# Performance work log

Hardware: AMD Instinct MI355X
Metric: run time of the kernel (lower is better)

## Reference

```python
import jax, jax.numpy as jnp
import numpy as np
from jax import lax

SEQ, B, IN, H, NLAYERS, OUT_LEN, OUT_SIZE = 80, 32768, 2, 10, 2, 20, 2


def _lstm_layer(x, h0, c0, Wih, Whh, bih, bhh):
    """PyTorch-convention LSTM layer. x: [T,B,F], h0/c0: [B,H]. Returns [T,B,H]."""
    b = bih + bhh  # [4H]

    def step(carry, xt):
        h, c = carry
        gates = xt @ Wih.T + h @ Whh.T + b  # [B,4H], gate order i,f,g,o
        i, f, g, o = jnp.split(gates, 4, axis=-1)
        i = jax.nn.sigmoid(i)
        f = jax.nn.sigmoid(f)
        g = jnp.tanh(g)
        o = jax.nn.sigmoid(o)
        c = f * c + i * g
        h = o * jnp.tanh(c)
        return (h, c), h

    (_, _), ys = lax.scan(step, (h0, c0), x)
    return ys


def setup_inputs() -> dict:
    key = jax.random.key(0)
    ks = jax.random.split(key, 16)
    s = 1.0 / np.sqrt(H)  # torch default init scale
    u = lambda k, shp: jax.random.uniform(k, shp, jnp.float32, -s, s)
    inp = {
        "x": jax.random.normal(ks[0], (SEQ, B, IN), jnp.float32),
        "h0": jnp.zeros((NLAYERS, B, H), jnp.float32),
        "c0": jnp.zeros((NLAYERS, B, H), jnp.float32),
        # layer 0 LSTM params
        "Wih0": u(ks[1], (4 * H, IN)),
        "Whh0": u(ks[2], (4 * H, H)),
        "bih0": u(ks[3], (4 * H,)),
        "bhh0": u(ks[4], (4 * H,)),
        # layer 1 LSTM params
        "Wih1": u(ks[5], (4 * H, H)),
        "Whh1": u(ks[6], (4 * H, H)),
        "bih1": u(ks[7], (4 * H,)),
        "bhh1": u(ks[8], (4 * H,)),
        # MLP head: Linear(800 -> 10), Sigmoid, Linear(10 -> 40)
        "W1": jax.random.uniform(ks[9], (H, SEQ * H), jnp.float32, -1 / np.sqrt(SEQ * H), 1 / np.sqrt(SEQ * H)),
        "b1": jax.random.uniform(ks[10], (H,), jnp.float32, -1 / np.sqrt(SEQ * H), 1 / np.sqrt(SEQ * H)),
        "W2": u(ks[11], (OUT_LEN * OUT_SIZE, H)),
        "b2": u(ks[12], (OUT_LEN * OUT_SIZE,)),
    }
    return inp


def reference(x, h0, c0, Wih0, Whh0, bih0, bhh0, Wih1, Whh1, bih1, bhh1, W1, b1, W2, b2):
    y0 = _lstm_layer(x, h0[0], c0[0], Wih0, Whh0, bih0, bhh0)   # [T,B,H]
    y1 = _lstm_layer(y0, h0[1], c0[1], Wih1, Whh1, bih1, bhh1)  # [T,B,H]
    out = jnp.tanh(y1)
    out = out.reshape(B, -1)  # faithful to torch .view(batch, -1) on [T,B,H]
    out = jax.nn.sigmoid(out @ W1.T + b1)
    out = out @ W2.T + b2  # [B, OUT_LEN*OUT_SIZE]
    return out.reshape(OUT_LEN, B, OUT_SIZE)
```

## Files before the change

kernel.cpp:

```cpp
#include <hip/hip_runtime.h>
#include <hip/hip_fp16.h>

#define SEQ   80
#define BATCH 32768
#define HID   10

typedef unsigned int uint;
typedef unsigned short ushort;
typedef _Float16 f16;
typedef __attribute__((ext_vector_type(8))) _Float16 f16x8;
typedef __attribute__((ext_vector_type(2))) _Float16 f16x2;
typedef __attribute__((ext_vector_type(4))) float f32x4;

#define SIG_SCALE  (-1.44269504f)
#define TANH_SCALE (-2.88539008f)

__device__ __forceinline__ float fast_rcp(float x)  { return __builtin_amdgcn_rcpf(x); }
__device__ __forceinline__ float fast_exp2(float x) { return __builtin_amdgcn_exp2f(x); }
__device__ __forceinline__ float sigp(float a)  { return fast_rcp(1.0f + fast_exp2(a)); }
__device__ __forceinline__ float tanhp(float a) { return 2.0f * fast_rcp(1.0f + fast_exp2(a)) - 1.0f; }
__device__ __forceinline__ float tanh_f(float x){ return tanhp(TANH_SCALE * x); }

union U4V { uint4 u; f16x8 v; };
union UH2 { uint u; f16x2 h; };
union HU  { f16 h; ushort s; };

__device__ __forceinline__ float lstm_unit(const f32x4 d, float& c) {
    const float Ei = fast_exp2(d[0]);
    const float Ef = fast_exp2(d[1]);
    const float Eg = fast_exp2(d[2]);
    const float Eo = fast_exp2(d[3]);
    const float Rf  = fast_rcp(1.0f + Ef);
    const float Rig = fast_rcp((1.0f + Ei) * (1.0f + Eg));
    c = c * Rf + (1.0f - Eg) * Rig;
    const float Ec = fast_exp2(TANH_SCALE * c);
    const float Rh = fast_rcp((1.0f + Eo) * (1.0f + Ec));
    return (1.0f - Ec) * Rh;
}

__global__ __launch_bounds__(256, 2)
void lstm2_mfma(const float* __restrict__ x, const float* __restrict__ h0in,
                const float* __restrict__ c0in,
                const float* __restrict__ Wih0, const float* __restrict__ Whh0,
                const float* __restrict__ bih0, const float* __restrict__ bhh0,
                const float* __restrict__ Wih1, const float* __restrict__ Whh1,
                const float* __restrict__ bih1, const float* __restrict__ bhh1,
                ushort* __restrict__ y ) {
    __shared__ char lds_all[4 * 16 * 80];
    const int tid = threadIdx.x;
    const int l   = tid & 63;
    const int wv  = tid >> 6;
    char* lds   = lds_all + wv * (16 * 80);
    const int bl  = l & 15;
    const int grp = l >> 4;
    const long b  = ((long)blockIdx.x * 4 + wv) * 16 + bl;

    f16x8 A0[3], A1[3];
    f32x4 bs0[3], bs1[3];
#pragma unroll
    for (int T = 0; T < 3; ++T) {
        const int R  = 16 * T + bl;
        const int u  = R >> 2, gi = R & 3;
        const bool vr = (R < 40);
        const int tr = gi * 10 + u;
        const float sc = (gi == 2) ? TANH_SCALE : SIG_SCALE;
#pragma unroll
        for (int j = 0; j < 8; ++j) {
            const int k = grp * 8 + j;
            float w0 = 0.f, w1 = 0.f;
            if (vr) {
                if (k < 10)      w0 = Whh0[tr * 10 + k];
                else if (k < 12) w0 = Wih0[tr * 2 + (k - 10)];
                if (k < 10)      w1 = Wih1[tr * 10 + k];
                else if (k < 20) w1 = Whh1[tr * 10 + (k - 10)];
            }
            A0[T][j] = (f16)(w0 * sc);
            A1[T][j] = (f16)(w1 * sc);
        }
#pragma unroll
        for (int q = 0; q < 4; ++q) {
            const int Rc = 16 * T + grp * 4 + q;
            const int uc = Rc >> 2, gc = Rc & 3;
            const float scc = (gc == 2) ? TANH_SCALE : SIG_SCALE;
            const int trc = gc * 10 + uc;
            bs0[T][q] = (Rc < 40) ? (bih0[trc] + bhh0[trc]) * scc : 0.f;
            bs1[T][q] = (Rc < 40) ? (bih1[trc] + bhh1[trc]) * scc : 0.f;
        }
    }

    float c0s[3], c1s[3];
#pragma unroll
    for (int T = 0; T < 3; ++T) {
        const int u = 4 * T + grp;
        const bool v = (u < 10);
        c0s[T] = v ? c0in[b * 10 + u] : 0.f;
        c1s[T] = v ? c0in[(size_t)BATCH * 10 + b * 10 + u] : 0.f;
    }

    {
        uint* p = (uint*)(lds) + l * 5;
#pragma unroll
        for (int i = 0; i < 5; ++i) p[i] = 0u;
    }
    char* myrow = lds + bl * 80;
#pragma unroll
    for (int T = 0; T < 3; ++T) {
        const int u = 4 * T + grp;
        if (u < 10) {
            *(f16*)(myrow + u * 2)      = (f16)h0in[b * 10 + u];
            *(f16*)(myrow + 20 + u * 2) = (f16)h0in[(size_t)BATCH * 10 + b * 10 + u];
        }
    }

    float h0nA, h0nB, h0nC;
    {
        const float2 xv = *reinterpret_cast<const float2*>(&x[b * 2]);
        U4V r0; r0.u = *reinterpret_cast<const uint4*>(myrow + (grp ? 16 : 0));
        UH2 xp; xp.h[0] = (f16)xv.x; xp.h[1] = (f16)xv.y;
        U4V b0v;
        b0v.u.x = (grp < 2)  ? r0.u.x : 0u;
        b0v.u.y = (grp == 0) ? r0.u.y : ((grp == 1) ? xp.u : 0u);
        b0v.u.z = (grp == 0) ? r0.u.z : 0u;
        b0v.u.w = (grp == 0) ? r0.u.w : 0u;
        f32x4 e0 = __builtin_amdgcn_mfma_f32_16x16x32_f16(A0[0], b0v.v, bs0[0], 0, 0, 0);
        f32x4 e1 = __builtin_amdgcn_mfma_f32_16x16x32_f16(A0[1], b0v.v, bs0[1], 0, 0, 0);
        f32x4 e2 = __builtin_amdgcn_mfma_f32_16x16x32_f16(A0[2], b0v.v, bs0[2], 0, 0, 0);
        h0nA = lstm_unit(e0, c0s[0]);
        h0nB = lstm_unit(e1, c0s[1]);
        h0nC = lstm_unit(e2, c0s[2]);
    }

    float2 xf = *reinterpret_cast<const float2*>(&x[((size_t)(SEQ > 1 ? 1 : 0) * BATCH + b) * 2]);

    for (int t = 0; t < SEQ; ++t) {
        const int tp = (t + 2 < SEQ) ? t + 2 : SEQ - 1;
        const float2 xpre = *reinterpret_cast<const float2*>(&x[((size_t)tp * BATCH + b) * 2]);

        *(f16*)(myrow + grp * 2)       = (f16)h0nA;
        *(f16*)(myrow + (4 + grp) * 2) = (f16)h0nB;
        if (grp < 2) *(f16*)(myrow + (8 + grp) * 2) = (f16)h0nC;

        U4V r1; r1.u = *reinterpret_cast<const uint4*>(myrow + grp * 16);
        U4V r0; r0.u = *reinterpret_cast<const uint4*>(myrow + (grp ? 16 : 0));

        UH2 xp; xp.h[0] = (f16)xf.x; xp.h[1] = (f16)xf.y;
        U4V b0v;
        b0v.u.x = (grp < 2)  ? r0.u.x : 0u;
        b0v.u.y = (grp == 0) ? r0.u.y : ((grp == 1) ? xp.u : 0u);
        b0v.u.z = (grp == 0) ? r0.u.z : 0u;
        b0v.u.w = (grp == 0) ? r0.u.w : 0u;

        f32x4 d0 = __builtin_amdgcn_mfma_f32_16x16x32_f16(A1[0], r1.v, bs1[0], 0, 0, 0);
        f32x4 d1 = __builtin_amdgcn_mfma_f32_16x16x32_f16(A1[1], r1.v, bs1[1], 0, 0, 0);
        f32x4 d2 = __builtin_amdgcn_mfma_f32_16x16x32_f16(A1[2], r1.v, bs1[2], 0, 0, 0);
        f32x4 e0 = __builtin_amdgcn_mfma_f32_16x16x32_f16(A0[0], b0v.v, bs0[0], 0, 0, 0);
        f32x4 e1 = __builtin_amdgcn_mfma_f32_16x16x32_f16(A0[1], b0v.v, bs0[1], 0, 0, 0);
        f32x4 e2 = __builtin_amdgcn_mfma_f32_16x16x32_f16(A0[2], b0v.v, bs0[2], 0, 0, 0);

        const float h1A = lstm_unit(d0, c1s[0]);
        const float h1B = lstm_unit(d1, c1s[1]);
        const float h1C = lstm_unit(d2, c1s[2]);
        h0nA = lstm_unit(e0, c0s[0]);
        h0nB = lstm_unit(e1, c0s[1]);
        h0nC = lstm_unit(e2, c0s[2]);

        HU hA; hA.h = (f16)h1A;
        HU hB; hB.h = (f16)h1B;
        HU hC; hC.h = (f16)h1C;
        *(f16*)(myrow + 20 + grp * 2)       = hA.h;
        *(f16*)(myrow + 20 + (4 + grp) * 2) = hB.h;
        if (grp < 2) *(f16*)(myrow + 20 + (8 + grp) * 2) = hC.h;

        ushort* yp = y + (size_t)t * BATCH * HID + b * HID;
        yp[grp] = hA.s;
        yp[4 + grp] = hB.s;
        if (grp < 2) yp[8 + grp] = hC.s;

        xf = xpre;
    }
}

__global__ __launch_bounds__(256, 2)
void head_mfma(const ushort* __restrict__ yflat,
               const float* __restrict__ W1, const float* __restrict__ b1,
               const float* __restrict__ W2, const float* __restrict__ b2,
               float* __restrict__ out) {
    __shared__ float sbuf[4][16][12];
    const int tid = threadIdx.x;
    const int l   = tid & 63;
    const int wv  = tid >> 6;
    const int bl  = l & 15;
    const int grp = l >> 4;
    const long row = ((long)blockIdx.x * 4 + wv) * 16 + bl;

    const ushort* yrow = yflat + row * 800;
    const float* arow = W1 + (size_t)(bl < 10 ? bl : 9) * 800;

    f32x4 acc = {0.f, 0.f, 0.f, 0.f};
#pragma unroll 5
    for (int c = 0; c < 25; ++c) {
        U4V bv; bv.u = *reinterpret_cast<const uint4*>(yrow + c * 32 + grp * 8);
        f16x8 tv;
#pragma unroll
        for (int e = 0; e < 8; ++e)
            tv[e] = (f16)tanh_f((float)bv.v[e]);
        const float4 w0 = *reinterpret_cast<const float4*>(arow + c * 32 + grp * 8);
        const float4 w1 = *reinterpret_cast<const float4*>(arow + c * 32 + grp * 8 + 4);
        f16x8 af;
        af[0] = (f16)w0.x; af[1] = (f16)w0.y; af[2] = (f16)w0.z; af[3] = (f16)w0.w;
        af[4] = (f16)w1.x; af[5] = (f16)w1.y; af[6] = (f16)w1.z; af[7] = (f16)w1.w;
        acc = __builtin_amdgcn_mfma_f32_16x16x32_f16(af, tv, acc, 0, 0, 0);
    }

#pragma unroll
    for (int q = 0; q < 4; ++q) {
        const int o = grp * 4 + q;
        if (o < 10)
            sbuf[wv][bl][o] = sigp(SIG_SCALE * (acc[q] + b1[o]));
    }

    float s[10];
#pragma unroll
    for (int o = 0; o < 10; ++o) s[o] = sbuf[wv][bl][o];

    float* op = out + row * 40 + grp * 10;
#pragma unroll
    for (int jj = 0; jj < 10; ++jj) {
        const int j = grp * 10 + jj;
        float r = b2[j];
#pragma unroll
        for (int o = 0; o < 10; ++o) r += s[o] * W2[j * 10 + o];
        op[jj] = r;
    }
}

extern "C" void kernel_launch(void* const* d_in, const int* in_sizes, int n_in,
                              void* d_out, int out_size, void* d_ws, size_t ws_size,
                              hipStream_t stream) {
    const float* x    = (const float*)d_in[0];
    const float* h0   = (const float*)d_in[1];
    const float* c0   = (const float*)d_in[2];
    const float* Wih0 = (const float*)d_in[3];
    const float* Whh0 = (const float*)d_in[4];
    const float* bih0 = (const float*)d_in[5];
    const float* bhh0 = (const float*)d_in[6];
    const float* Wih1 = (const float*)d_in[7];
    const float* Whh1 = (const float*)d_in[8];
    const float* bih1 = (const float*)d_in[9];
    const float* bhh1 = (const float*)d_in[10];
    const float* W1   = (const float*)d_in[11];
    const float* b1   = (const float*)d_in[12];
    const float* W2   = (const float*)d_in[13];
    const float* b2   = (const float*)d_in[14];
    float* out = (float*)d_out;
    ushort* yws = (ushort*)d_ws;

    lstm2_mfma<<<512, 256, 0, stream>>>(x, h0, c0, Wih0, Whh0, bih0, bhh0,
                                        Wih1, Whh1, bih1, bhh1, yws);
    head_mfma<<<512, 256, 0, stream>>>(yws, W1, b1, W2, b2, out);
}
```

Baseline: 104.5 us.

## Split LSTM layers across paired wavefronts with triple-buffered LDS handoff

Each batch tile of 16 rows now gets two wavefronts: one runs layer 0 and the other runs layer 1, which lags by one timestep. The two exchange hidden states through a triple-buffered LDS ring, with a block barrier each step. This halves the per-wave register footprint and doubles the wave count (1024 blocks, launch bounds 4), so latency can be hidden across more waves. The cost is a __syncthreads every step, one extra pipeline step, and threads left idle at the first and last steps.

```diff
diff --git a/kernel.cpp b/kernel.cpp
--- a/kernel.cpp
+++ b/kernel.cpp
@@ -38,25 +38,26 @@
     return (1.0f - Ec) * Rh;
 }
 
-__global__ __launch_bounds__(256, 2)
-void lstm2_mfma(const float* __restrict__ x, const float* __restrict__ h0in,
+__global__ __launch_bounds__(256, 4)
+void lstm2_spec(const float* __restrict__ x, const float* __restrict__ h0in,
                 const float* __restrict__ c0in,
                 const float* __restrict__ Wih0, const float* __restrict__ Whh0,
                 const float* __restrict__ bih0, const float* __restrict__ bhh0,
                 const float* __restrict__ Wih1, const float* __restrict__ Whh1,
                 const float* __restrict__ bih1, const float* __restrict__ bhh1,
                 ushort* __restrict__ y ) {
-    __shared__ char lds_all[4 * 16 * 80];
-    const int tid = threadIdx.x;
-    const int l   = tid & 63;
-    const int wv  = tid >> 6;
-    char* lds   = lds_all + wv * (16 * 80);
-    const int bl  = l & 15;
-    const int grp = l >> 4;
-    const long b  = ((long)blockIdx.x * 4 + wv) * 16 + bl;
-
-    f16x8 A0[3], A1[3];
-    f32x4 bs0[3], bs1[3];
+    __shared__ __align__(16) ushort buf[2][3][16][40];
+    const int tid  = threadIdx.x;
+    const int l    = tid & 63;
+    const int wv   = tid >> 6;
+    const int pair = wv >> 1;
+    const int role = wv & 1;
+    const int bl   = l & 15;
+    const int grp  = l >> 4;
+    const long b   = ((long)blockIdx.x * 2 + pair) * 16 + bl;
+
+    f16x8 A[3];
+    f32x4 bs[3];
 #pragma unroll
     for (int T = 0; T < 3; ++T) {
         const int R  = 16 * T + bl;
@@ -67,15 +68,17 @@
 #pragma unroll
         for (int j = 0; j < 8; ++j) {
             const int k = grp * 8 + j;
-            float w0 = 0.f, w1 = 0.f;
+            float w = 0.f;
             if (vr) {
-                if (k < 10)      w0 = Whh0[tr * 10 + k];
-                else if (k < 12) w0 = Wih0[tr * 2 + (k - 10)];
-                if (k < 10)      w1 = Wih1[tr * 10 + k];
-                else if (k < 20) w1 = Whh1[tr * 10 + (k - 10)];
+                if (role == 0) {
+                    if (k < 10)      w = Whh0[tr * 10 + k];
+                    else if (k < 12) w = Wih0[tr * 2 + (k - 10)];
+                } else {
+                    if (k < 10)      w = Wih1[tr * 10 + k];
+                    else if (k < 20) w = Whh1[tr * 10 + (k - 10)];
+                }
             }
-            A0[T][j] = (f16)(w0 * sc);
-            A1[T][j] = (f16)(w1 * sc);
+            A[T][j] = (f16)(w * sc);
         }
 #pragma unroll
         for (int q = 0; q < 4; ++q) {
@@ -83,100 +86,101 @@
             const int uc = Rc >> 2, gc = Rc & 3;
             const float scc = (gc == 2) ? TANH_SCALE : SIG_SCALE;
             const int trc = gc * 10 + uc;
-            bs0[T][q] = (Rc < 40) ? (bih0[trc] + bhh0[trc]) * scc : 0.f;
-            bs1[T][q] = (Rc < 40) ? (bih1[trc] + bhh1[trc]) * scc : 0.f;
-        }
-    }
-
-    float c0s[3], c1s[3];
+            float bb = 0.f;
+            if (Rc < 40)
+                bb = (role == 0) ? (bih0[trc] + bhh0[trc]) : (bih1[trc] + bhh1[trc]);
+            bs[T][q] = bb * scc;
+        }
+    }
+
+    const size_t cbase = (role == 0) ? 0 : (size_t)BATCH * 10;
+    float cS[3];
 #pragma unroll
     for (int T = 0; T < 3; ++T) {
         const int u = 4 * T + grp;
-        const bool v = (u < 10);
-        c0s[T] = v ? c0in[b * 10 + u] : 0.f;
-        c1s[T] = v ? c0in[(size_t)BATCH * 10 + b * 10 + u] : 0.f;
+        cS[T] = (u < 10) ? c0in[cbase + b * 10 + u] : 0.f;
     }
 
     {
-        uint* p = (uint*)(lds) + l * 5;
-#pragma unroll
-        for (int i = 0; i < 5; ++i) p[i] = 0u;
-    }
-    char* myrow = lds + bl * 80;
-#pragma unroll
-    for (int T = 0; T < 3; ++T) {
-        const int u = 4 * T + grp;
-        if (u < 10) {
-            *(f16*)(myrow + u * 2)      = (f16)h0in[b * 10 + u];
-            *(f16*)(myrow + 20 + u * 2) = (f16)h0in[(size_t)BATCH * 10 + b * 10 + u];
-        }
-    }
-
-    float h0nA, h0nB, h0nC;
-    {
-        const float2 xv = *reinterpret_cast<const float2*>(&x[b * 2]);
-        U4V r0; r0.u = *reinterpret_cast<const uint4*>(myrow + (grp ? 16 : 0));
-        UH2 xp; xp.h[0] = (f16)xv.x; xp.h[1] = (f16)xv.y;
-        U4V b0v;
-        b0v.u.x = (grp < 2)  ? r0.u.x : 0u;
-        b0v.u.y = (grp == 0) ? r0.u.y : ((grp == 1) ? xp.u : 0u);
-        b0v.u.z = (grp == 0) ? r0.u.z : 0u;
-        b0v.u.w = (grp == 0) ? r0.u.w : 0u;
-        f32x4 e0 = __builtin_amdgcn_mfma_f32_16x16x32_f16(A0[0], b0v.v, bs0[0], 0, 0, 0);
-        f32x4 e1 = __builtin_amdgcn_mfma_f32_16x16x32_f16(A0[1], b0v.v, bs0[1], 0, 0, 0);
-        f32x4 e2 = __builtin_amdgcn_mfma_f32_16x16x32_f16(A0[2], b0v.v, bs0[2], 0, 0, 0);
-        h0nA = lstm_unit(e0, c0s[0]);
-        h0nB = lstm_unit(e1, c0s[1]);
-        h0nC = lstm_unit(e2, c0s[2]);
-    }
-
-    float2 xf = *reinterpret_cast<const float2*>(&x[((size_t)(SEQ > 1 ? 1 : 0) * BATCH + b) * 2]);
-
-    for (int t = 0; t < SEQ; ++t) {
-        const int tp = (t + 2 < SEQ) ? t + 2 : SEQ - 1;
-        const float2 xpre = *reinterpret_cast<const float2*>(&x[((size_t)tp * BATCH + b) * 2]);
-
-        *(f16*)(myrow + grp * 2)       = (f16)h0nA;
-        *(f16*)(myrow + (4 + grp) * 2) = (f16)h0nB;
-        if (grp < 2) *(f16*)(myrow + (8 + grp) * 2) = (f16)h0nC;
-
-        U4V r1; r1.u = *reinterpret_cast<const uint4*>(myrow + grp * 16);
-        U4V r0; r0.u = *reinterpret_cast<const uint4*>(myrow + (grp ? 16 : 0));
-
-        UH2 xp; xp.h[0] = (f16)xf.x; xp.h[1] = (f16)xf.y;
-        U4V b0v;
-        b0v.u.x = (grp < 2)  ? r0.u.x : 0u;
-        b0v.u.y = (grp == 0) ? r0.u.y : ((grp == 1) ? xp.u : 0u);
-        b0v.u.z = (grp == 0) ? r0.u.z : 0u;
-        b0v.u.w = (grp == 0) ? r0.u.w : 0u;
-
-        f32x4 d0 = __builtin_amdgcn_mfma_f32_16x16x32_f16(A1[0], r1.v, bs1[0], 0, 0, 0);
-        f32x4 d1 = __builtin_amdgcn_mfma_f32_16x16x32_f16(A1[1], r1.v, bs1[1], 0, 0, 0);
-        f32x4 d2 = __builtin_amdgcn_mfma_f32_16x16x32_f16(A1[2], r1.v, bs1[2], 0, 0, 0);
-        f32x4 e0 = __builtin_amdgcn_mfma_f32_16x16x32_f16(A0[0], b0v.v, bs0[0], 0, 0, 0);
-        f32x4 e1 = __builtin_amdgcn_mfma_f32_16x16x32_f16(A0[1], b0v.v, bs0[1], 0, 0, 0);
-        f32x4 e2 = __builtin_amdgcn_mfma_f32_16x16x32_f16(A0[2], b0v.v, bs0[2], 0, 0, 0);
-
-        const float h1A = lstm_unit(d0, c1s[0]);
-        const float h1B = lstm_unit(d1, c1s[1]);
-        const float h1C = lstm_unit(d2, c1s[2]);
-        h0nA = lstm_unit(e0, c0s[0]);
-        h0nB = lstm_unit(e1, c0s[1]);
-        h0nC = lstm_unit(e2, c0s[2]);
-
-        HU hA; hA.h = (f16)h1A;
-        HU hB; hB.h = (f16)h1B;
-        HU hC; hC.h = (f16)h1C;
-        *(f16*)(myrow + 20 + grp * 2)       = hA.h;
-        *(f16*)(myrow + 20 + (4 + grp) * 2) = hB.h;
-        if (grp < 2) *(f16*)(myrow + 20 + (8 + grp) * 2) = hC.h;
-
-        ushort* yp = y + (size_t)t * BATCH * HID + b * HID;
-        yp[grp] = hA.s;
-        yp[4 + grp] = hB.s;
-        if (grp < 2) yp[8 + grp] = hC.s;
-
-        xf = xpre;
+        uint* p = (uint*)buf;
+        for (int idx = tid; idx < 1920; idx += 256) p[idx] = 0u;
+    }
+    __syncthreads();
+    if (role == 0) {
+        ushort* row = &buf[pair][2][bl][0];
+#pragma unroll
+        for (int T = 0; T < 3; ++T) {
+            const int u = 4 * T + grp;
+            if (u < 10) { HU h; h.h = (f16)h0in[b * 10 + u]; row[u] = h.s; }
+        }
+    } else {
+        ushort* row = &buf[pair][0][bl][0];
+#pragma unroll
+        for (int T = 0; T < 3; ++T) {
+            const int u = 4 * T + grp;
+            if (u < 10) { HU h; h.h = (f16)h0in[(size_t)BATCH * 10 + b * 10 + u]; row[10 + u] = h.s; }
+        }
+    }
+
+    float2 xv = make_float2(0.f, 0.f);
+    if (role == 0) xv = *reinterpret_cast<const float2*>(&x[b * 2]);
+
+    for (int i = 0; i <= SEQ; ++i) {
+        __syncthreads();
+        const int wq = i % 3;
+        const int rq = (i + 2) % 3;
+        const ushort* rrow = &buf[pair][rq][bl][0];
+        ushort* wrow = &buf[pair][wq][bl][0];
+
+        if (role == 0) {
+            if (i < SEQ) {
+                const int tn = (i + 1 < SEQ) ? i + 1 : SEQ - 1;
+                const float2 xnext = *reinterpret_cast<const float2*>(&x[((size_t)tn * BATCH + b) * 2]);
+
+                U4V r; r.u = *reinterpret_cast<const uint4*>(rrow + grp * 8);
+                UH2 xp; xp.h[0] = (f16)xv.x; xp.h[1] = (f16)xv.y;
+                U4V bv;
+                bv.u.x = (grp < 2)  ? r.u.x : 0u;
+                bv.u.y = (grp == 0) ? r.u.y : ((grp == 1) ? xp.u : 0u);
+                bv.u.z = (grp == 0) ? r.u.z : 0u;
+                bv.u.w = (grp == 0) ? r.u.w : 0u;
+
+                f32x4 d0 = __builtin_amdgcn_mfma_f32_16x16x32_f16(A[0], bv.v, bs[0], 0, 0, 0);
+                f32x4 d1 = __builtin_amdgcn_mfma_f32_16x16x32_f16(A[1], bv.v, bs[1], 0, 0, 0);
+                f32x4 d2 = __builtin_amdgcn_mfma_f32_16x16x32_f16(A[2], bv.v, bs[2], 0, 0, 0);
+
+                HU hA; hA.h = (f16)lstm_unit(d0, cS[0]);
+                HU hB; hB.h = (f16)lstm_unit(d1, cS[1]);
+                HU hC; hC.h = (f16)lstm_unit(d2, cS[2]);
+
+                wrow[grp] = hA.s;
+                wrow[4 + grp] = hB.s;
+                if (grp < 2) wrow[8 + grp] = hC.s;
+
+                xv = xnext;
+            }
+        } else {
+            if (i >= 1) {
+                U4V r; r.u = *reinterpret_cast<const uint4*>(rrow + grp * 8);
+
+                f32x4 d0 = __builtin_amdgcn_mfma_f32_16x16x32_f16(A[0], r.v, bs[0], 0, 0, 0);
+                f32x4 d1 = __builtin_amdgcn_mfma_f32_16x16x32_f16(A[1], r.v, bs[1], 0, 0, 0);
+                f32x4 d2 = __builtin_amdgcn_mfma_f32_16x16x32_f16(A[2], r.v, bs[2], 0, 0, 0);
+
+                HU hA; hA.h = (f16)lstm_unit(d0, cS[0]);
+                HU hB; hB.h = (f16)lstm_unit(d1, cS[1]);
+                HU hC; hC.h = (f16)lstm_unit(d2, cS[2]);
+
+                wrow[10 + grp] = hA.s;
+                wrow[14 + grp] = hB.s;
+                if (grp < 2) wrow[18 + grp] = hC.s;
+
+                ushort* yp = y + (size_t)(i - 1) * BATCH * HID + b * HID;
+                yp[grp] = hA.s;
+                yp[4 + grp] = hB.s;
+                if (grp < 2) yp[8 + grp] = hC.s;
+            }
+        }
     }
 }
 
@@ -255,7 +259,7 @@
     float* out = (float*)d_out;
     ushort* yws = (ushort*)d_ws;
 
-    lstm2_mfma<<<512, 256, 0, stream>>>(x, h0, c0, Wih0, Whh0, bih0, bhh0,
-                                        Wih1, Whh1, bih1, bhh1, yws);
+    lstm2_spec<<<1024, 256, 0, stream>>>(x, h0, c0, Wih0, Whh0, bih0, bhh0,
+                                         Wih1, Whh1, bih1, bhh1, yws);
     head_mfma<<<512, 256, 0, stream>>>(yws, W1, b1, W2, b2, out);
 }
```

New measurement: 104.9 us. Within noise of the previous version (+0.4%).
